# Kernel tuning notes

Hardware: AMD Instinct MI355X
Metric: run time of the kernel (lower is better)

The kernel has to match this reference:

```python
import jax, jax.numpy as jnp
import numpy as np

STRIDES = (8, 16, 32, 64, 128)
POOL = 7
IMG = 1024.0


def _crop_and_resize(fm, boxes, box_ids, crop_h, crop_w):
    """tf.image.crop_and_resize semantics (bilinear, extrapolation_value=0).
    fm: [B,H,W,C] channels-last; boxes: [N,4] normalized (y1,x1,y2,x2); box_ids: [N] int.
    Returns [N,crop_h,crop_w,C]."""
    B, H, W, C = fm.shape
    y1, x1, y2, x2 = boxes[:, 0], boxes[:, 1], boxes[:, 2], boxes[:, 3]
    fy = jnp.arange(crop_h, dtype=boxes.dtype) / (crop_h - 1)
    fx = jnp.arange(crop_w, dtype=boxes.dtype) / (crop_w - 1)
    ys = (y1[:, None] + (y2 - y1)[:, None] * fy) * (H - 1)   # [N,crop_h]
    xs = (x1[:, None] + (x2 - x1)[:, None] * fx) * (W - 1)   # [N,crop_w]
    y0f = jnp.floor(ys)
    x0f = jnp.floor(xs)
    wy = (ys - y0f)[:, :, None, None]
    wx = (xs - x0f)[:, None, :, None]
    y0 = jnp.clip(y0f, 0, H - 1).astype(jnp.int32)
    y1i = jnp.clip(y0f + 1, 0, H - 1).astype(jnp.int32)
    x0 = jnp.clip(x0f, 0, W - 1).astype(jnp.int32)
    x1i = jnp.clip(x0f + 1, 0, W - 1).astype(jnp.int32)
    b = box_ids[:, None, None]
    gather = lambda yi, xi: fm[b, yi[:, :, None], xi[:, None, :]]  # [N,ch,cw,C]
    top = gather(y0, x0) * (1 - wx) + gather(y0, x1i) * wx
    bot = gather(y1i, x0) * (1 - wx) + gather(y1i, x1i) * wx
    out = top * (1 - wy) + bot * wy
    valid = ((ys >= 0) & (ys <= H - 1))[:, :, None] & ((xs >= 0) & (xs <= W - 1))[:, None, :]
    return jnp.where(valid[..., None], out, jnp.zeros((), out.dtype))


def reference(batch_gt_boxes, fm0, fm1, fm2, fm3, fm4):
    boxes = batch_gt_boxes[..., :4]
    B, N, _ = boxes.shape
    box_ids = jnp.repeat(jnp.arange(B, dtype=jnp.int32), N)  # [B*N]
    boxes = boxes.reshape(-1, 4)
    # trim_padding_boxes: inputs contain no all-zero (padding) boxes, so all kept.
    rois_from_fms = []
    for fm, s in zip((fm0, fm1, fm2, fm3, fm4), STRIDES):
        H, W = fm.shape[1], fm.shape[2]
        # normalize_boxes: pixel coords -> feature-map coords (/stride) -> [0,1]
        scale = jnp.array([s * (H - 1), s * (W - 1), s * (H - 1), s * (W - 1)],
                          dtype=boxes.dtype)
        normed = boxes / scale
        rois_from_fms.append(_crop_and_resize(fm, normed, box_ids, POOL, POOL))
    rois = jnp.concatenate(rois_from_fms, axis=-1)  # [B*N, 7, 7, 5*C]
    return rois, box_ids


def setup_inputs() -> dict:
    key = jax.random.key(0)
    ks = jax.random.split(key, 6)
    u = jax.random.uniform(ks[0], (8, 100, 4), dtype=jnp.float32) * IMG
    ya, xa, yb, xb = u[..., 0], u[..., 1], u[..., 2], u[..., 3]
    # valid, non-degenerate, non-zero boxes (so trim_padding_boxes keeps all)
    batch_gt_boxes = jnp.stack([
        jnp.minimum(ya, yb), jnp.minimum(xa, xb),
        jnp.maximum(ya, yb) + 1.0, jnp.maximum(xa, xb) + 1.0], axis=-1)
    fms = {}
    for i, s in enumerate(STRIDES):
        hw = int(IMG) // s
        fms[f"fm{i}"] = jax.random.normal(ks[i + 1], (8, hw, hw, 256), dtype=jnp.float32)
    return {"batch_gt_boxes": batch_gt_boxes, **fms}
```

## Files before the change

kernel.cpp:

```cpp
#include <hip/hip_runtime.h>

#define NCH 256
#define ROIS_ELEMS 50176000

typedef float vf2 __attribute__((ext_vector_type(2)));

__global__ __launch_bounds__(256) void roi_row_kernel(
    const float* __restrict__ boxes,
    const float* __restrict__ fm0,
    const float* __restrict__ fm1,
    const float* __restrict__ fm2,
    const float* __restrict__ fm3,
    const float* __restrict__ fm4,
    float* __restrict__ out,
    float* __restrict__ out_ids)
{
    const int wave = threadIdx.x >> 6;
    const int lane = threadIdx.x & 63;

    const int bswz = (blockIdx.x & 7) * 1750 + (blockIdx.x >> 3);
    const int wg   = bswz * 4 + wave;
    const int row  = wg >> 1;
    const int half = wg & 1;

    const int n   = row / 35;
    const int rem = row - n * 35;
    const int l   = rem / 7;
    const int py  = rem - l * 7;

    const float* fm;
    switch (l) {
        case 0: fm = fm0; break;
        case 1: fm = fm1; break;
        case 2: fm = fm2; break;
        case 3: fm = fm3; break;
        default: fm = fm4; break;
    }
    const int H = 128 >> l;
    const float Hm1 = (float)(H - 1);
    const float scale = (float)((8 << l) * (H - 1));

    const int img = n / 100;
    const float y1 = boxes[n * 4 + 0];
    const float x1 = boxes[n * 4 + 1];
    const float y2 = boxes[n * 4 + 2];
    const float x2 = boxes[n * 4 + 3];

    const float y1n = __fdiv_rn(y1, scale);
    const float y2n = __fdiv_rn(y2, scale);
    const float x1n = __fdiv_rn(x1, scale);
    const float x2n = __fdiv_rn(x2, scale);

    const float fy = __fdiv_rn((float)py, 6.0f);
    const float ys = __fmul_rn(__fadd_rn(y1n, __fmul_rn(__fsub_rn(y2n, y1n), fy)), Hm1);
    const bool  vy = (ys >= 0.0f) && (ys <= Hm1);
    const float y0f = floorf(ys);
    const float wy  = ys - y0f;
    const float owy = 1.0f - wy;
    const int y0  = (int)fminf(fmaxf(y0f,        0.0f), Hm1);
    const int y1i = (int)fminf(fmaxf(y0f + 1.0f, 0.0f), Hm1);

    const int rowTop = (img * H + y0 ) * H;
    const int rowBot = (img * H + y1i) * H;
    const int chOff  = half * 128;

    float wx_[7];
    bool  vx_[7];
    int oT0[7], oT1[7], oB0[7], oB1[7];
    #pragma unroll
    for (int px = 0; px < 7; ++px) {
        const float fx = __fdiv_rn((float)px, 6.0f);
        const float xs = __fmul_rn(__fadd_rn(x1n, __fmul_rn(__fsub_rn(x2n, x1n), fx)), Hm1);
        vx_[px] = (xs >= 0.0f) && (xs <= Hm1);
        const float x0f = floorf(xs);
        wx_[px] = xs - x0f;
        const int x0  = (int)fminf(fmaxf(x0f,        0.0f), Hm1);
        const int x1i = (int)fminf(fmaxf(x0f + 1.0f, 0.0f), Hm1);
        oT0[px] = __builtin_amdgcn_readfirstlane((rowTop + x0 ) * NCH + chOff);
        oT1[px] = __builtin_amdgcn_readfirstlane((rowTop + x1i) * NCH + chOff);
        oB0[px] = __builtin_amdgcn_readfirstlane((rowBot + x0 ) * NCH + chOff);
        oB1[px] = __builtin_amdgcn_readfirstlane((rowBot + x1i) * NCH + chOff);
    }

    vf2 v00[7], v01[7], v10[7], v11[7];
    #pragma unroll
    for (int px = 0; px < 7; ++px) {
        v00[px] = ((const vf2*)(fm + oT0[px]))[lane];
        v01[px] = ((const vf2*)(fm + oT1[px]))[lane];
        v10[px] = ((const vf2*)(fm + oB0[px]))[lane];
        v11[px] = ((const vf2*)(fm + oB1[px]))[lane];
    }

    float* obase = out + ((n * 7 + py) * 7) * 1280 + l * NCH + chOff;
    #pragma unroll
    for (int px = 0; px < 7; ++px) {
        const float wx  = wx_[px];
        const float owx = 1.0f - wx;
        vf2 r = (v00[px] * owx + v01[px] * wx) * owy
              + (v10[px] * owx + v11[px] * wx) * wy;
        if (!(vy && vx_[px])) { r = (vf2)0.0f; }
        __builtin_nontemporal_store(r, ((vf2*)(obase + px * 1280)) + lane);
    }

    if (l == 0 && py == 0 && half == 0 && lane == 0) {
        out_ids[n] = (float)img;
    }
}

extern "C" void kernel_launch(void* const* d_in, const int* in_sizes, int n_in,
                              void* d_out, int out_size, void* d_ws, size_t ws_size,
                              hipStream_t stream) {
    const float* boxes = (const float*)d_in[0];
    const float* fm0   = (const float*)d_in[1];
    const float* fm1   = (const float*)d_in[2];
    const float* fm2   = (const float*)d_in[3];
    const float* fm3   = (const float*)d_in[4];
    const float* fm4   = (const float*)d_in[5];

    float* out     = (float*)d_out;
    float* out_ids = out + ROIS_ELEMS;

    roi_row_kernel<<<14000, 256, 0, stream>>>(boxes, fm0, fm1, fm2, fm3, fm4, out, out_ids);
}
```

Baseline: 68.87 us.

## Process whole box per wave and reuse bilinear source rows across output rows

Each wave now handles all seven crop rows of one box/level/channel-half instead of a single row, keeping the two loaded source rows in registers. When consecutive crop rows map to the same feature-map rows, those loads are skipped or shifted instead of reissued. This reduces redundant gather traffic, especially on coarse levels, but cuts the grid sevenfold and serializes rows within a wave, which lowers memory-level parallelism.

```diff
diff --git a/kernel.cpp b/kernel.cpp
--- a/kernel.cpp
+++ b/kernel.cpp
@@ -5,7 +5,7 @@
 
 typedef float vf2 __attribute__((ext_vector_type(2)));
 
-__global__ __launch_bounds__(256) void roi_row_kernel(
+__global__ __launch_bounds__(256) void roi_box_kernel(
     const float* __restrict__ boxes,
     const float* __restrict__ fm0,
     const float* __restrict__ fm1,
@@ -18,15 +18,13 @@
     const int wave = threadIdx.x >> 6;
     const int lane = threadIdx.x & 63;
 
-    const int bswz = (blockIdx.x & 7) * 1750 + (blockIdx.x >> 3);
+    const int bswz = (blockIdx.x & 7) * 250 + (blockIdx.x >> 3);
     const int wg   = bswz * 4 + wave;
-    const int row  = wg >> 1;
-    const int half = wg & 1;
 
-    const int n   = row / 35;
-    const int rem = row - n * 35;
-    const int l   = rem / 7;
-    const int py  = rem - l * 7;
+    const int n    = wg / 10;
+    const int rem  = wg - n * 10;
+    const int l    = rem >> 1;
+    const int half = rem & 1;
 
     const float* fm;
     switch (l) {
@@ -40,7 +38,9 @@
     const float Hm1 = (float)(H - 1);
     const float scale = (float)((8 << l) * (H - 1));
 
-    const int img = n / 100;
+    const int img   = n / 100;
+    const int chOff = half * 128;
+
     const float y1 = boxes[n * 4 + 0];
     const float x1 = boxes[n * 4 + 1];
     const float y2 = boxes[n * 4 + 2];
@@ -51,22 +51,9 @@
     const float x1n = __fdiv_rn(x1, scale);
     const float x2n = __fdiv_rn(x2, scale);
 
-    const float fy = __fdiv_rn((float)py, 6.0f);
-    const float ys = __fmul_rn(__fadd_rn(y1n, __fmul_rn(__fsub_rn(y2n, y1n), fy)), Hm1);
-    const bool  vy = (ys >= 0.0f) && (ys <= Hm1);
-    const float y0f = floorf(ys);
-    const float wy  = ys - y0f;
-    const float owy = 1.0f - wy;
-    const int y0  = (int)fminf(fmaxf(y0f,        0.0f), Hm1);
-    const int y1i = (int)fminf(fmaxf(y0f + 1.0f, 0.0f), Hm1);
-
-    const int rowTop = (img * H + y0 ) * H;
-    const int rowBot = (img * H + y1i) * H;
-    const int chOff  = half * 128;
-
     float wx_[7];
     bool  vx_[7];
-    int oT0[7], oT1[7], oB0[7], oB1[7];
+    int c0[7], c1[7];
     #pragma unroll
     for (int px = 0; px < 7; ++px) {
         const float fx = __fdiv_rn((float)px, 6.0f);
@@ -76,33 +63,74 @@
         wx_[px] = xs - x0f;
         const int x0  = (int)fminf(fmaxf(x0f,        0.0f), Hm1);
         const int x1i = (int)fminf(fmaxf(x0f + 1.0f, 0.0f), Hm1);
-        oT0[px] = __builtin_amdgcn_readfirstlane((rowTop + x0 ) * NCH + chOff);
-        oT1[px] = __builtin_amdgcn_readfirstlane((rowTop + x1i) * NCH + chOff);
-        oB0[px] = __builtin_amdgcn_readfirstlane((rowBot + x0 ) * NCH + chOff);
-        oB1[px] = __builtin_amdgcn_readfirstlane((rowBot + x1i) * NCH + chOff);
+        c0[px] = __builtin_amdgcn_readfirstlane(x0  * NCH + chOff);
+        c1[px] = __builtin_amdgcn_readfirstlane(x1i * NCH + chOff);
     }
 
-    vf2 v00[7], v01[7], v10[7], v11[7];
+    vf2 A0[7], A1[7], B0[7], B1[7];
+    int curA = -1, curB = -1;
+
     #pragma unroll
-    for (int px = 0; px < 7; ++px) {
-        v00[px] = ((const vf2*)(fm + oT0[px]))[lane];
-        v01[px] = ((const vf2*)(fm + oT1[px]))[lane];
-        v10[px] = ((const vf2*)(fm + oB0[px]))[lane];
-        v11[px] = ((const vf2*)(fm + oB1[px]))[lane];
+    for (int py = 0; py < 7; ++py) {
+        const float fy = __fdiv_rn((float)py, 6.0f);
+        const float ys = __fmul_rn(__fadd_rn(y1n, __fmul_rn(__fsub_rn(y2n, y1n), fy)), Hm1);
+        const bool  vy = (ys >= 0.0f) && (ys <= Hm1);
+        const float y0f = floorf(ys);
+        const float wy  = ys - y0f;
+        const float owy = 1.0f - wy;
+        const int y0  = __builtin_amdgcn_readfirstlane(
+                            (int)fminf(fmaxf(y0f,        0.0f), Hm1));
+        const int y1i = __builtin_amdgcn_readfirstlane(
+                            (int)fminf(fmaxf(y0f + 1.0f, 0.0f), Hm1));
+
+        const int oA = __builtin_amdgcn_readfirstlane((img * H + y0 ) * H * NCH);
+        const int oB = __builtin_amdgcn_readfirstlane((img * H + y1i) * H * NCH);
+
+        if (y0 == curA) {
+            if (y1i != curB) {
+                #pragma unroll
+                for (int px = 0; px < 7; ++px) {
+                    B0[px] = ((const vf2*)(fm + oB + c0[px]))[lane];
+                    B1[px] = ((const vf2*)(fm + oB + c1[px]))[lane];
+                }
+            }
+        } else if (y0 == curB) {
+            #pragma unroll
+            for (int px = 0; px < 7; ++px) { A0[px] = B0[px]; A1[px] = B1[px]; }
+            if (y1i != curB) {
+                #pragma unroll
+                for (int px = 0; px < 7; ++px) {
+                    B0[px] = ((const vf2*)(fm + oB + c0[px]))[lane];
+                    B1[px] = ((const vf2*)(fm + oB + c1[px]))[lane];
+                }
+            }
+        } else {
+            #pragma unroll
+            for (int px = 0; px < 7; ++px) {
+                A0[px] = ((const vf2*)(fm + oA + c0[px]))[lane];
+                A1[px] = ((const vf2*)(fm + oA + c1[px]))[lane];
+            }
+            #pragma unroll
+            for (int px = 0; px < 7; ++px) {
+                B0[px] = ((const vf2*)(fm + oB + c0[px]))[lane];
+                B1[px] = ((const vf2*)(fm + oB + c1[px]))[lane];
+            }
+        }
+        curA = y0; curB = y1i;
+
+        float* obase = out + ((n * 7 + py) * 7) * 1280 + l * NCH + chOff;
+        #pragma unroll
+        for (int px = 0; px < 7; ++px) {
+            const float wx  = wx_[px];
+            const float owx = 1.0f - wx;
+            vf2 r = (A0[px] * owx + A1[px] * wx) * owy
+                  + (B0[px] * owx + B1[px] * wx) * wy;
+            if (!(vy && vx_[px])) { r = (vf2)0.0f; }
+            __builtin_nontemporal_store(r, ((vf2*)(obase + px * 1280)) + lane);
+        }
     }
 
-    float* obase = out + ((n * 7 + py) * 7) * 1280 + l * NCH + chOff;
-    #pragma unroll
-    for (int px = 0; px < 7; ++px) {
-        const float wx  = wx_[px];
-        const float owx = 1.0f - wx;
-        vf2 r = (v00[px] * owx + v01[px] * wx) * owy
-              + (v10[px] * owx + v11[px] * wx) * wy;
-        if (!(vy && vx_[px])) { r = (vf2)0.0f; }
-        __builtin_nontemporal_store(r, ((vf2*)(obase + px * 1280)) + lane);
-    }
-
-    if (l == 0 && py == 0 && half == 0 && lane == 0) {
+    if (l == 0 && half == 0 && lane == 0) {
         out_ids[n] = (float)img;
     }
 }
@@ -120,5 +148,5 @@
     float* out     = (float*)d_out;
     float* out_ids = out + ROIS_ELEMS;
 
-    roi_row_kernel<<<14000, 256, 0, stream>>>(boxes, fm0, fm1, fm2, fm3, fm4, out, out_ids);
+    roi_box_kernel<<<2000, 256, 0, stream>>>(boxes, fm0, fm1, fm2, fm3, fm4, out, out_ids);
 }
```

Result: no change. 70.09 us (+1.8%).
